# Kernel tuning notes

Measured on AMD Instinct MI355X. Metric: run time of the kernel, lower is better.

Reference implementation:

```python
import jax, jax.numpy as jnp
import numpy as np

B, H, W, C = 32, 112, 112, 192
SE_RATIO, CBAM_RATIO = 16, 8


def setup_inputs() -> dict:
    key = jax.random.key(0)
    ks = jax.random.split(key, 8)
    s = lambda fan_in: 1.0 / np.sqrt(fan_in)
    x = jax.random.normal(ks[0], (B, H, W, C), dtype=jnp.float32)
    se_w1 = jax.random.normal(ks[1], (C, C // SE_RATIO), dtype=jnp.float32) * s(C)
    se_b1 = jnp.zeros((C // SE_RATIO,), jnp.float32)
    se_w2 = jax.random.normal(ks[2], (C // SE_RATIO, C), dtype=jnp.float32) * s(C // SE_RATIO)
    se_b2 = jnp.zeros((C,), jnp.float32)
    mlp_w1 = jax.random.normal(ks[3], (C, C // CBAM_RATIO), dtype=jnp.float32) * s(C)
    mlp_b1 = jnp.zeros((C // CBAM_RATIO,), jnp.float32)
    mlp_w2 = jax.random.normal(ks[4], (C // CBAM_RATIO, C), dtype=jnp.float32) * s(C // CBAM_RATIO)
    mlp_b2 = jnp.zeros((C,), jnp.float32)
    conv_k = jax.random.normal(ks[5], (7, 7, 2, 1), dtype=jnp.float32) * s(7 * 7 * 2)  # HWIO
    conv_b = jnp.zeros((1,), jnp.float32)
    return {"x": x, "se_w1": se_w1, "se_b1": se_b1, "se_w2": se_w2, "se_b2": se_b2,
            "mlp_w1": mlp_w1, "mlp_b1": mlp_b1, "mlp_w2": mlp_w2, "mlp_b2": mlp_b2,
            "conv_k": conv_k, "conv_b": conv_b}


def _swish(v):
    return v * jax.nn.sigmoid(v)


def reference(x, se_w1, se_b1, se_w2, se_b2, mlp_w1, mlp_b1, mlp_w2, mlp_b2, conv_k, conv_b):
    # ---- pooled channel stats (B, C) ----
    avg_pool = jnp.mean(x, axis=(1, 2))
    max_pool = jnp.max(x, axis=(1, 2))

    # ---- SE branch: Dense(swish) -> Dense(sigmoid) on global avg ----
    se = _swish(avg_pool @ se_w1 + se_b1)
    se = jax.nn.sigmoid(se @ se_w2 + se_b2)           # (B, C)
    se = se[:, None, None, :]                          # (B,1,1,C)

    # ---- CBAM channel attention: shared MLP on avg+max, sigmoid of sum ----
    def mlp(v):
        return _swish(v @ mlp_w1 + mlp_b1) @ mlp_w2 + mlp_b2
    channel_att = jax.nn.sigmoid(mlp(avg_pool) + mlp(max_pool))  # (B, C)
    channel_att = channel_att[:, None, None, :]

    # ---- CBAM spatial attention: 7x7 conv on [mean_c, max_c] maps ----
    avg_sp = jnp.mean(x, axis=-1, keepdims=True)       # (B,H,W,1)
    max_sp = jnp.max(x, axis=-1, keepdims=True)        # (B,H,W,1)
    concat = jnp.concatenate([avg_sp, max_sp], axis=-1)  # (B,H,W,2)
    spatial = jax.lax.conv_general_dilated(
        concat, conv_k, window_strides=(1, 1), padding="SAME",
        dimension_numbers=("NHWC", "HWIO", "NHWC"))
    spatial_att = jax.nn.sigmoid(spatial + conv_b)      # (B,H,W,1)

    return x * se * channel_att * spatial_att
```

## Files before the change

kernel.cpp:

```cpp
#include <hip/hip_runtime.h>

#define B_   32
#define H_   112
#define W_   112
#define C_   192
#define HW_  (H_*W_)
#define BC_  (B_*C_)
#define NPIX (B_*HW_)
#define NF4  (B_*HW_*C_/4)

__device__ __forceinline__ float sigmoidf_(float v) {
    return 1.0f / (1.0f + __expf(-v));
}

__device__ __forceinline__ unsigned f2mono(float f) {
    unsigned u = __float_as_uint(f);
    return (u & 0x80000000u) ? ~u : (u | 0x80000000u);
}
__device__ __forceinline__ float mono2f(unsigned u) {
    return __uint_as_float((u & 0x80000000u) ? (u & 0x7FFFFFFFu) : ~u);
}

__global__ __launch_bounds__(256) void k_init(float* gsum, unsigned* gmax) {
    int i = blockIdx.x * 256 + threadIdx.x;
    if (i < BC_) { gsum[i] = 0.0f; gmax[i] = 0u; }
}

__global__ __launch_bounds__(256) void k_pool(const float* __restrict__ x,
                                              float* __restrict__ gsum,
                                              unsigned* __restrict__ gmax,
                                              float* __restrict__ avg_sp,
                                              float* __restrict__ max_sp) {
    const int t   = threadIdx.x;
    const int row = blockIdx.x;
    const int b   = row / H_;
    const float4* xr = (const float4*)(x + (size_t)row * (W_ * C_));

    float4 s4 = {0.f, 0.f, 0.f, 0.f};
    float4 m4 = {-3.0e38f, -3.0e38f, -3.0e38f, -3.0e38f};
    const int c4 = t % 48;
    const int g  = t / 48;
    if (t < 240) {
        for (int p = g; p < W_; p += 5) {
            float4 v = xr[p * 48 + c4];
            s4.x += v.x; s4.y += v.y; s4.z += v.z; s4.w += v.w;
            m4.x = fmaxf(m4.x, v.x); m4.y = fmaxf(m4.y, v.y);
            m4.z = fmaxf(m4.z, v.z); m4.w = fmaxf(m4.w, v.w);
        }
    }

    const int sub = t & 15;
    const int pg  = t >> 4;
    for (int k = 0; k < 7; ++k) {
        const int p = pg + 16 * k;
        float4 a = xr[p * 48 + sub];
        float4 c = xr[p * 48 + sub + 16];
        float4 d = xr[p * 48 + sub + 32];
        float s = (a.x + a.y + a.z + a.w) + (c.x + c.y + c.z + c.w) + (d.x + d.y + d.z + d.w);
        float m = fmaxf(fmaxf(fmaxf(a.x, a.y), fmaxf(a.z, a.w)),
                 fmaxf(fmaxf(fmaxf(c.x, c.y), fmaxf(c.z, c.w)),
                       fmaxf(fmaxf(d.x, d.y), fmaxf(d.z, d.w))));
        #pragma unroll
        for (int sh = 1; sh < 16; sh <<= 1) {
            s += __shfl_xor(s, sh, 64);
            m = fmaxf(m, __shfl_xor(m, sh, 64));
        }
        if (sub == 0) {
            const int pix = row * W_ + p;
            avg_sp[pix] = s * (1.0f / C_);
            max_sp[pix] = m;
        }
    }

    __shared__ float4 ls[240];
    __shared__ float4 lm[240];
    if (t < 240) { ls[t] = s4; lm[t] = m4; }
    __syncthreads();
    if (t < 48) {
        float4 S = ls[t], M = lm[t];
        #pragma unroll
        for (int gg = 1; gg < 5; ++gg) {
            float4 o = ls[t + 48 * gg];
            S.x += o.x; S.y += o.y; S.z += o.z; S.w += o.w;
            float4 om = lm[t + 48 * gg];
            M.x = fmaxf(M.x, om.x); M.y = fmaxf(M.y, om.y);
            M.z = fmaxf(M.z, om.z); M.w = fmaxf(M.w, om.w);
        }
        float* gs = gsum + b * C_ + t * 4;
        atomicAdd(gs + 0, S.x); atomicAdd(gs + 1, S.y);
        atomicAdd(gs + 2, S.z); atomicAdd(gs + 3, S.w);
        unsigned* gm = gmax + b * C_ + t * 4;
        atomicMax(gm + 0, f2mono(M.x)); atomicMax(gm + 1, f2mono(M.y));
        atomicMax(gm + 2, f2mono(M.z)); atomicMax(gm + 3, f2mono(M.w));
    }
}

__global__ __launch_bounds__(192) void k_small(const float* __restrict__ gsum,
                                               const unsigned* __restrict__ gmax,
                                               const float* __restrict__ se_w1,
                                               const float* __restrict__ se_b1,
                                               const float* __restrict__ se_w2,
                                               const float* __restrict__ se_b2,
                                               const float* __restrict__ mlp_w1,
                                               const float* __restrict__ mlp_b1,
                                               const float* __restrict__ mlp_w2,
                                               const float* __restrict__ mlp_b2,
                                               float* __restrict__ scale) {
    const int b = blockIdx.x, t = threadIdx.x;
    __shared__ float avg[C_], mx[C_], hse[12], ha[24], hm[24];
    avg[t] = gsum[b * C_ + t] * (1.0f / HW_);
    mx[t]  = mono2f(gmax[b * C_ + t]);
    __syncthreads();
    if (t < 12) {
        float z = se_b1[t];
        for (int c = 0; c < C_; ++c) z += avg[c] * se_w1[c * 12 + t];
        hse[t] = z * sigmoidf_(z);
    }
    if (t < 24) {
        float za = mlp_b1[t], zm = mlp_b1[t];
        for (int c = 0; c < C_; ++c) {
            float w = mlp_w1[c * 24 + t];
            za += avg[c] * w;
            zm += mx[c] * w;
        }
        ha[t] = za * sigmoidf_(za);
        hm[t] = zm * sigmoidf_(zm);
    }
    __syncthreads();
    float sv = se_b2[t];
    #pragma unroll
    for (int j = 0; j < 12; ++j) sv += hse[j] * se_w2[j * C_ + t];
    float av = 2.0f * mlp_b2[t];
    #pragma unroll
    for (int j = 0; j < 24; ++j) av += (ha[j] + hm[j]) * mlp_w2[j * C_ + t];
    scale[b * C_ + t] = sigmoidf_(sv) * sigmoidf_(av);
}

__global__ __launch_bounds__(256) void k_conv(const float* __restrict__ avg_sp,
                                              const float* __restrict__ max_sp,
                                              const float* __restrict__ conv_k,
                                              const float* __restrict__ conv_b,
                                              float* __restrict__ satt) {
    __shared__ float lk[98];
    __shared__ float lb;
    const int t = threadIdx.x;
    if (t < 98) lk[t] = conv_k[t];
    if (t == 0) lb = conv_b[0];
    __syncthreads();
    const int idx = blockIdx.x * 256 + t;
    if (idx >= NPIX) return;
    const int b  = idx / HW_;
    const int r  = idx % HW_;
    const int y  = r / W_;
    const int x0 = r % W_;
    const float* ab = avg_sp + b * HW_;
    const float* mb = max_sp + b * HW_;
    float acc = lb;
    #pragma unroll
    for (int dy = 0; dy < 7; ++dy) {
        const int yy = y + dy - 3;
        if (yy < 0 || yy >= H_) continue;
        #pragma unroll
        for (int dx = 0; dx < 7; ++dx) {
            const int xx = x0 + dx - 3;
            if (xx < 0 || xx >= W_) continue;
            const int o = yy * W_ + xx;
            acc += ab[o] * lk[(dy * 7 + dx) * 2] + mb[o] * lk[(dy * 7 + dx) * 2 + 1];
        }
    }
    satt[idx] = sigmoidf_(acc);
}

__global__ __launch_bounds__(256) void k_apply(const float4* __restrict__ x4,
                                               const float* __restrict__ scale,
                                               const float* __restrict__ satt,
                                               float4* __restrict__ out4) {
    const int idx = blockIdx.x * 256 + threadIdx.x;
    if (idx >= NF4) return;
    const int pix = idx / 48;
    const int c4  = idx - pix * 48;
    const int b   = pix / HW_;
    const float ss = satt[pix];
    const float4 sc = ((const float4*)scale)[b * 48 + c4];
    float4 v = x4[idx];
    float4 o;
    o.x = v.x * sc.x * ss;
    o.y = v.y * sc.y * ss;
    o.z = v.z * sc.z * ss;
    o.w = v.w * sc.w * ss;
    out4[idx] = o;
}

extern "C" void kernel_launch(void* const* d_in, const int* in_sizes, int n_in,
                              void* d_out, int out_size, void* d_ws, size_t ws_size,
                              hipStream_t stream) {
    const float* x      = (const float*)d_in[0];
    const float* se_w1  = (const float*)d_in[1];
    const float* se_b1  = (const float*)d_in[2];
    const float* se_w2  = (const float*)d_in[3];
    const float* se_b2  = (const float*)d_in[4];
    const float* mlp_w1 = (const float*)d_in[5];
    const float* mlp_b1 = (const float*)d_in[6];
    const float* mlp_w2 = (const float*)d_in[7];
    const float* mlp_b2 = (const float*)d_in[8];
    const float* conv_k = (const float*)d_in[9];
    const float* conv_b = (const float*)d_in[10];
    float* out = (float*)d_out;

    float*    ws     = (float*)d_ws;
    float*    gsum   = ws;
    unsigned* gmax   = (unsigned*)(ws + 6144);
    float*    scale  = ws + 12288;
    float*    avg_sp = ws + 18432;
    float*    max_sp = ws + 419840;
    float*    satt   = ws + 821248;

    k_init <<<(BC_ + 255) / 256, 256, 0, stream>>>(gsum, gmax);
    k_pool <<<B_ * H_, 256, 0, stream>>>(x, gsum, gmax, avg_sp, max_sp);
    k_small<<<B_, 192, 0, stream>>>(gsum, gmax, se_w1, se_b1, se_w2, se_b2,
                                    mlp_w1, mlp_b1, mlp_w2, mlp_b2, scale);
    k_conv <<<(NPIX + 255) / 256, 256, 0, stream>>>(avg_sp, max_sp, conv_k, conv_b, satt);
    k_apply<<<NF4 / 256, 256, 0, stream>>>((const float4*)x, scale, satt, (float4*)out);
}
```

Measured before the change: 644.0 us.

## Fuse spatial conv into apply, single-pass pooling with per-row partials instead of atomics

The pooling kernel now accumulates per-channel sum and max from the same loads used for the per-pixel channel stats, so each row of x is read once. It writes per-row partials instead of global atomics, which also removes the init kernel; the small kernel reduces these over rows. The 7x7 spatial conv is computed inside the apply kernel from a shared-memory halo, one block per image row, which drops a separate kernel and the attention buffer. The trade-off is extra shared-memory staging and more partial-sum workspace.

```diff
diff --git a/kernel.cpp b/kernel.cpp
--- a/kernel.cpp
+++ b/kernel.cpp
@@ -7,96 +7,83 @@
 #define HW_  (H_*W_)
 #define BC_  (B_*C_)
 #define NPIX (B_*HW_)
-#define NF4  (B_*HW_*C_/4)
+#define NROW (B_*H_)
+#define C4_  (C_/4)
 
 __device__ __forceinline__ float sigmoidf_(float v) {
     return 1.0f / (1.0f + __expf(-v));
 }
 
-__device__ __forceinline__ unsigned f2mono(float f) {
-    unsigned u = __float_as_uint(f);
-    return (u & 0x80000000u) ? ~u : (u | 0x80000000u);
-}
-__device__ __forceinline__ float mono2f(unsigned u) {
-    return __uint_as_float((u & 0x80000000u) ? (u & 0x7FFFFFFFu) : ~u);
-}
-
-__global__ __launch_bounds__(256) void k_init(float* gsum, unsigned* gmax) {
-    int i = blockIdx.x * 256 + threadIdx.x;
-    if (i < BC_) { gsum[i] = 0.0f; gmax[i] = 0u; }
-}
-
 __global__ __launch_bounds__(256) void k_pool(const float* __restrict__ x,
-                                              float* __restrict__ gsum,
-                                              unsigned* __restrict__ gmax,
+                                              float* __restrict__ psum,
+                                              float* __restrict__ pmax,
                                               float* __restrict__ avg_sp,
                                               float* __restrict__ max_sp) {
     const int t   = threadIdx.x;
     const int row = blockIdx.x;
-    const int b   = row / H_;
     const float4* xr = (const float4*)(x + (size_t)row * (W_ * C_));
-
-    float4 s4 = {0.f, 0.f, 0.f, 0.f};
-    float4 m4 = {-3.0e38f, -3.0e38f, -3.0e38f, -3.0e38f};
-    const int c4 = t % 48;
-    const int g  = t / 48;
-    if (t < 240) {
-        for (int p = g; p < W_; p += 5) {
-            float4 v = xr[p * 48 + c4];
-            s4.x += v.x; s4.y += v.y; s4.z += v.z; s4.w += v.w;
-            m4.x = fmaxf(m4.x, v.x); m4.y = fmaxf(m4.y, v.y);
-            m4.z = fmaxf(m4.z, v.z); m4.w = fmaxf(m4.w, v.w);
-        }
-    }
 
     const int sub = t & 15;
     const int pg  = t >> 4;
+
+    float4 s0 = {0.f,0.f,0.f,0.f}, s1 = s0, s2 = s0;
+    const float NEG = -3.0e38f;
+    float4 m0 = {NEG,NEG,NEG,NEG}, m1 = m0, m2 = m0;
+
+    #pragma unroll
     for (int k = 0; k < 7; ++k) {
         const int p = pg + 16 * k;
-        float4 a = xr[p * 48 + sub];
-        float4 c = xr[p * 48 + sub + 16];
-        float4 d = xr[p * 48 + sub + 32];
+        float4 a = xr[p * C4_ + sub];
+        float4 c = xr[p * C4_ + sub + 16];
+        float4 d = xr[p * C4_ + sub + 32];
+
+        s0.x += a.x; s0.y += a.y; s0.z += a.z; s0.w += a.w;
+        s1.x += c.x; s1.y += c.y; s1.z += c.z; s1.w += c.w;
+        s2.x += d.x; s2.y += d.y; s2.z += d.z; s2.w += d.w;
+        m0.x = fmaxf(m0.x, a.x); m0.y = fmaxf(m0.y, a.y);
+        m0.z = fmaxf(m0.z, a.z); m0.w = fmaxf(m0.w, a.w);
+        m1.x = fmaxf(m1.x, c.x); m1.y = fmaxf(m1.y, c.y);
+        m1.z = fmaxf(m1.z, c.z); m1.w = fmaxf(m1.w, c.w);
+        m2.x = fmaxf(m2.x, d.x); m2.y = fmaxf(m2.y, d.y);
+        m2.z = fmaxf(m2.z, d.z); m2.w = fmaxf(m2.w, d.w);
+
         float s = (a.x + a.y + a.z + a.w) + (c.x + c.y + c.z + c.w) + (d.x + d.y + d.z + d.w);
         float m = fmaxf(fmaxf(fmaxf(a.x, a.y), fmaxf(a.z, a.w)),
                  fmaxf(fmaxf(fmaxf(c.x, c.y), fmaxf(c.z, c.w)),
-                       fmaxf(fmaxf(d.x, d.y), fmaxf(d.z, d.w))));
+                       fmaxf(fmaxf(fmaxf(d.x, d.y), fmaxf(d.z, d.w)), NEG)));
         #pragma unroll
         for (int sh = 1; sh < 16; sh <<= 1) {
             s += __shfl_xor(s, sh, 64);
             m = fmaxf(m, __shfl_xor(m, sh, 64));
         }
         if (sub == 0) {
-            const int pix = row * W_ + p;
-            avg_sp[pix] = s * (1.0f / C_);
-            max_sp[pix] = m;
-        }
-    }
-
-    __shared__ float4 ls[240];
-    __shared__ float4 lm[240];
-    if (t < 240) { ls[t] = s4; lm[t] = m4; }
-    __syncthreads();
-    if (t < 48) {
-        float4 S = ls[t], M = lm[t];
+            avg_sp[row * W_ + p] = s * (1.0f / C_);
+            max_sp[row * W_ + p] = m;
+        }
+    }
+
+    __shared__ float4 lsum[16][49];
+    __shared__ float4 lmax[16][49];
+    lsum[pg][sub]      = s0; lsum[pg][sub + 16] = s1; lsum[pg][sub + 32] = s2;
+    lmax[pg][sub]      = m0; lmax[pg][sub + 16] = m1; lmax[pg][sub + 32] = m2;
+    __syncthreads();
+    if (t < C4_) {
+        float4 S = lsum[0][t], M = lmax[0][t];
         #pragma unroll
-        for (int gg = 1; gg < 5; ++gg) {
-            float4 o = ls[t + 48 * gg];
+        for (int g = 1; g < 16; ++g) {
+            float4 o  = lsum[g][t];
             S.x += o.x; S.y += o.y; S.z += o.z; S.w += o.w;
-            float4 om = lm[t + 48 * gg];
+            float4 om = lmax[g][t];
             M.x = fmaxf(M.x, om.x); M.y = fmaxf(M.y, om.y);
             M.z = fmaxf(M.z, om.z); M.w = fmaxf(M.w, om.w);
         }
-        float* gs = gsum + b * C_ + t * 4;
-        atomicAdd(gs + 0, S.x); atomicAdd(gs + 1, S.y);
-        atomicAdd(gs + 2, S.z); atomicAdd(gs + 3, S.w);
-        unsigned* gm = gmax + b * C_ + t * 4;
-        atomicMax(gm + 0, f2mono(M.x)); atomicMax(gm + 1, f2mono(M.y));
-        atomicMax(gm + 2, f2mono(M.z)); atomicMax(gm + 3, f2mono(M.w));
-    }
-}
-
-__global__ __launch_bounds__(192) void k_small(const float* __restrict__ gsum,
-                                               const unsigned* __restrict__ gmax,
+        ((float4*)psum)[row * C4_ + t] = S;
+        ((float4*)pmax)[row * C4_ + t] = M;
+    }
+}
+
+__global__ __launch_bounds__(192) void k_small(const float* __restrict__ psum,
+                                               const float* __restrict__ pmax,
                                                const float* __restrict__ se_w1,
                                                const float* __restrict__ se_b1,
                                                const float* __restrict__ se_w2,
@@ -107,9 +94,17 @@
                                                const float* __restrict__ mlp_b2,
                                                float* __restrict__ scale) {
     const int b = blockIdx.x, t = threadIdx.x;
+    const float* ps = psum + (size_t)b * H_ * C_ + t;
+    const float* pm = pmax + (size_t)b * H_ * C_ + t;
+    float s = 0.f, m = -3.0e38f;
+    #pragma unroll 4
+    for (int h = 0; h < H_; ++h) {
+        s += ps[h * C_];
+        m = fmaxf(m, pm[h * C_]);
+    }
     __shared__ float avg[C_], mx[C_], hse[12], ha[24], hm[24];
-    avg[t] = gsum[b * C_ + t] * (1.0f / HW_);
-    mx[t]  = mono2f(gmax[b * C_ + t]);
+    avg[t] = s * (1.0f / HW_);
+    mx[t]  = m;
     __syncthreads();
     if (t < 12) {
         float z = se_b1[t];
@@ -136,64 +131,91 @@
     scale[b * C_ + t] = sigmoidf_(sv) * sigmoidf_(av);
 }
 
-__global__ __launch_bounds__(256) void k_conv(const float* __restrict__ avg_sp,
-                                              const float* __restrict__ max_sp,
-                                              const float* __restrict__ conv_k,
-                                              const float* __restrict__ conv_b,
-                                              float* __restrict__ satt) {
-    __shared__ float lk[98];
-    __shared__ float lb;
-    const int t = threadIdx.x;
-    if (t < 98) lk[t] = conv_k[t];
-    if (t == 0) lb = conv_b[0];
-    __syncthreads();
-    const int idx = blockIdx.x * 256 + t;
-    if (idx >= NPIX) return;
-    const int b  = idx / HW_;
-    const int r  = idx % HW_;
-    const int y  = r / W_;
-    const int x0 = r % W_;
-    const float* ab = avg_sp + b * HW_;
-    const float* mb = max_sp + b * HW_;
-    float acc = lb;
-    #pragma unroll
-    for (int dy = 0; dy < 7; ++dy) {
-        const int yy = y + dy - 3;
-        if (yy < 0 || yy >= H_) continue;
-        #pragma unroll
-        for (int dx = 0; dx < 7; ++dx) {
-            const int xx = x0 + dx - 3;
-            if (xx < 0 || xx >= W_) continue;
-            const int o = yy * W_ + xx;
-            acc += ab[o] * lk[(dy * 7 + dx) * 2] + mb[o] * lk[(dy * 7 + dx) * 2 + 1];
-        }
-    }
-    satt[idx] = sigmoidf_(acc);
-}
-
 __global__ __launch_bounds__(256) void k_apply(const float4* __restrict__ x4,
                                                const float* __restrict__ scale,
-                                               const float* __restrict__ satt,
+                                               const float* __restrict__ avg_sp,
+                                               const float* __restrict__ max_sp,
+                                               const float* __restrict__ conv_k,
+                                               const float* __restrict__ conv_b,
                                                float4* __restrict__ out4) {
-    const int idx = blockIdx.x * 256 + threadIdx.x;
-    if (idx >= NF4) return;
-    const int pix = idx / 48;
-    const int c4  = idx - pix * 48;
-    const int b   = pix / HW_;
-    const float ss = satt[pix];
-    const float4 sc = ((const float4*)scale)[b * 48 + c4];
-    float4 v = x4[idx];
-    float4 o;
-    o.x = v.x * sc.x * ss;
-    o.y = v.y * sc.y * ss;
-    o.z = v.z * sc.z * ss;
-    o.w = v.w * sc.w * ss;
-    out4[idx] = o;
+    const int t   = threadIdx.x;
+    const int row = blockIdx.x;
+    const int b   = row / H_;
+    const int y   = row - b * H_;
+
+    __shared__ float sA[7][118];
+    __shared__ float sM[7][118];
+    __shared__ float ssc[C_];
+    __shared__ float patt[2][112];
+    __shared__ float ssatt[112];
+
+    if (t < C_) ssc[t] = scale[b * C_ + t];
+
+    const float* ab = avg_sp + (size_t)b * HW_;
+    const float* mb = max_sp + (size_t)b * HW_;
+    for (int i = t; i < 7 * 118; i += 256) {
+        const int r  = i / 118;
+        const int cc = i - r * 118;
+        const int yy = y + r - 3;
+        const int xx = cc - 3;
+        float va = 0.f, vm = 0.f;
+        if (yy >= 0 && yy < H_ && xx >= 0 && xx < W_) {
+            va = ab[yy * W_ + xx];
+            vm = mb[yy * W_ + xx];
+        }
+        sA[r][cc] = va;
+        sM[r][cc] = vm;
+    }
+    __syncthreads();
+
+    const int half = t >> 7;
+    const int px   = t & 127;
+    if (px < 112) {
+        float acc = 0.f;
+        if (half == 0) {
+            #pragma unroll
+            for (int dy = 0; dy < 4; ++dy)
+                #pragma unroll
+                for (int dx = 0; dx < 7; ++dx)
+                    acc += sA[dy][px + dx] * conv_k[(dy * 7 + dx) * 2]
+                         + sM[dy][px + dx] * conv_k[(dy * 7 + dx) * 2 + 1];
+        } else {
+            #pragma unroll
+            for (int dy = 4; dy < 7; ++dy)
+                #pragma unroll
+                for (int dx = 0; dx < 7; ++dx)
+                    acc += sA[dy][px + dx] * conv_k[(dy * 7 + dx) * 2]
+                         + sM[dy][px + dx] * conv_k[(dy * 7 + dx) * 2 + 1];
+        }
+        patt[half][px] = acc;
+    }
+    __syncthreads();
+    if (t < 112) ssatt[t] = sigmoidf_(patt[0][t] + patt[1][t] + conv_b[0]);
+    __syncthreads();
+
+    const float4* xrow = x4   + (size_t)row * (W_ * C4_);
+    float4*       orow = out4 + (size_t)row * (W_ * C4_);
+    #pragma unroll
+    for (int i = 0; i < 21; ++i) {
+        const int idx = i * 256 + t;
+        const int pl  = idx / C4_;
+        const int c4  = idx - pl * C4_;
+        const float  ss = ssatt[pl];
+        const float4 sc = ((const float4*)ssc)[c4];
+        float4 v = xrow[idx];
+        float4 o;
+        o.x = v.x * sc.x * ss;
+        o.y = v.y * sc.y * ss;
+        o.z = v.z * sc.z * ss;
+        o.w = v.w * sc.w * ss;
+        orow[idx] = o;
+    }
 }
 
 extern "C" void kernel_launch(void* const* d_in, const int* in_sizes, int n_in,
                               void* d_out, int out_size, void* d_ws, size_t ws_size,
                               hipStream_t stream) {
+    (void)in_sizes; (void)n_in; (void)out_size; (void)ws_size;
     const float* x      = (const float*)d_in[0];
     const float* se_w1  = (const float*)d_in[1];
     const float* se_b1  = (const float*)d_in[2];
@@ -207,18 +229,16 @@
     const float* conv_b = (const float*)d_in[10];
     float* out = (float*)d_out;
 
-    float*    ws     = (float*)d_ws;
-    float*    gsum   = ws;
-    unsigned* gmax   = (unsigned*)(ws + 6144);
-    float*    scale  = ws + 12288;
-    float*    avg_sp = ws + 18432;
-    float*    max_sp = ws + 419840;
-    float*    satt   = ws + 821248;
-
-    k_init <<<(BC_ + 255) / 256, 256, 0, stream>>>(gsum, gmax);
-    k_pool <<<B_ * H_, 256, 0, stream>>>(x, gsum, gmax, avg_sp, max_sp);
-    k_small<<<B_, 192, 0, stream>>>(gsum, gmax, se_w1, se_b1, se_w2, se_b2,
+    float* ws     = (float*)d_ws;
+    float* psum   = ws;
+    float* pmax   = ws + 688128;
+    float* scale  = ws + 1376256;
+    float* avg_sp = ws + 1382400;
+    float* max_sp = ws + 1783808;
+
+    k_pool <<<NROW, 256, 0, stream>>>(x, psum, pmax, avg_sp, max_sp);
+    k_small<<<B_, 192, 0, stream>>>(psum, pmax, se_w1, se_b1, se_w2, se_b2,
                                     mlp_w1, mlp_b1, mlp_w2, mlp_b2, scale);
-    k_conv <<<(NPIX + 255) / 256, 256, 0, stream>>>(avg_sp, max_sp, conv_k, conv_b, satt);
-    k_apply<<<NF4 / 256, 256, 0, stream>>>((const float4*)x, scale, satt, (float4*)out);
-}
+    k_apply<<<NROW, 256, 0, stream>>>((const float4*)x, scale, avg_sp, max_sp,
+                                      conv_k, conv_b, (float4*)out);
+}
```

Result: faster. 603.1 us (-6.3%).
